# Optimization experiments

Measured on AMD Instinct MI355X. Metric: run time of the kernel, lower is better.

Reference implementation:

```python
import jax, jax.numpy as jnp
import numpy as np

N_HEAD = 9
HEAD_DIM = 64
KV_PER_HEAD = 21  # 189 // 9
ROPE_BASE = 10000.0


def _rotate_half(x):
    # matches torch: x1 = first half (floor), x2 = rest; cat(-x2, x1)
    h = x.shape[-1] // 2
    return jnp.concatenate([-x[..., h:], x[..., :h]], axis=-1)


def _rope_cos_sin(T, dtype):
    inv_freq = 1.0 / (ROPE_BASE ** (jnp.arange(0, KV_PER_HEAD, 2, dtype=jnp.float32) / KV_PER_HEAD))  # [11]
    t = jnp.arange(T, dtype=jnp.float32)
    freqs = jnp.einsum('i,j->ij', t, inv_freq)          # [T, 11]
    emb = jnp.concatenate([freqs, freqs], axis=-1)      # [T, 22]
    cos = jnp.cos(emb)[:, :KV_PER_HEAD].astype(dtype)   # [T, 21]
    sin = jnp.sin(emb)[:, :KV_PER_HEAD].astype(dtype)
    return cos, sin


def setup_inputs() -> dict:
    key = jax.random.key(0)
    ks = jax.random.split(key, 5)
    B, T, C = 4, 2048, 576
    kv_dim = 189
    s = 0.02
    return {
        'x': jax.random.normal(ks[0], (B, T, C), dtype=jnp.float32),
        'Wq': jax.random.normal(ks[1], (C, C), dtype=jnp.float32) * s,
        'Wk': jax.random.normal(ks[2], (C, kv_dim), dtype=jnp.float32) * s,
        'Wv': jax.random.normal(ks[3], (C, kv_dim), dtype=jnp.float32) * s,
        'Wo': jax.random.normal(ks[4], (C, C), dtype=jnp.float32) * s,
    }


def reference(x, Wq, Wk, Wv, Wo):
    B, T, C = x.shape
    q = (x @ Wq).reshape(B, T, N_HEAD, HEAD_DIM).transpose(0, 2, 1, 3)      # [B,H,T,64]
    k = (x @ Wk).reshape(B, T, N_HEAD, KV_PER_HEAD).transpose(0, 2, 1, 3)   # [B,H,T,21]
    v = (x @ Wv).reshape(B, T, N_HEAD, KV_PER_HEAD).transpose(0, 2, 1, 3)   # [B,H,T,21]

    cos, sin = _rope_cos_sin(T, x.dtype)  # [T,21] each, broadcasts over B,H
    k_rot = k * cos + _rotate_half(k) * sin
    q_part = q[..., :KV_PER_HEAD]
    q_rot_part = q_part * cos + _rotate_half(q_part) * sin
    # q dims >= KV_PER_HEAD never touch nonzero K, so only the first 21 dims matter
    scale = 1.0 / np.sqrt(HEAD_DIM)
    scores = jnp.einsum('bhqd,bhkd->bhqk', q_rot_part, k_rot) * scale       # [B,H,T,T]
    causal = jnp.tril(jnp.ones((T, T), dtype=bool))
    scores = jnp.where(causal, scores, -1e9)
    attn = jax.nn.softmax(scores, axis=-1)
    y_small = jnp.einsum('bhqk,bhkd->bhqd', attn, v)                        # [B,H,T,21]
    # zero-pad up to head_dim (matches k_pad/v_pad construction)
    y = jnp.pad(y_small, ((0, 0), (0, 0), (0, 0), (0, HEAD_DIM - KV_PER_HEAD)))
    y = y.transpose(0, 2, 1, 3).reshape(B, T, C)
    return y @ Wo
```

## Files before the change

kernel.cpp:

```cpp
#include <hip/hip_runtime.h>
#include <hip/hip_bf16.h>

typedef unsigned short u16;
typedef unsigned int u32;
typedef __attribute__((ext_vector_type(8))) short bf16x8;
typedef __attribute__((ext_vector_type(4))) float f32x4;
typedef __attribute__((ext_vector_type(4))) int i32x4;

#define N_HEADS 9
#define T_SEQ 2048
#define BATCH 4
#define CDIM 576
#define ROWS (BATCH * T_SEQ)
#define NBH (BATCH * N_HEADS)
#define PART_SLOT ((size_t)NBH * T_SEQ * 32)

__device__ __forceinline__ u16 f2bf(float f) {
    u32 u = __float_as_uint(f);
    u32 r = u + 0x7FFFu + ((u >> 16) & 1u);
    return (u16)(r >> 16);
}
__device__ __forceinline__ float bf2f(u16 u) { return __uint_as_float(((u32)u) << 16); }
__device__ __forceinline__ u32 cvt_pk_bf16(float lo, float hi) {
    u32 r;
    asm("v_cvt_pk_bf16_f32 %0, %1, %2" : "=v"(r) : "v"(lo), "v"(hi));
    return r;
}
__device__ __forceinline__ float exp2_raw(float x) {
    float r;
    asm("v_exp_f32 %0, %1" : "=v"(r) : "v"(x));
    return r;
}

__global__ __launch_bounds__(256) void prep_wt(const float* __restrict__ Wq, const float* __restrict__ Wk,
                                               const float* __restrict__ Wv, const float* __restrict__ Wo,
                                               u16* __restrict__ WcT, u16* __restrict__ WoSubT,
                                               float* __restrict__ cosT, float* __restrict__ sinT) {
    int idx = blockIdx.x * 256 + threadIdx.x;
    if (idx < 576 * 576) {
        int n = idx / 576, k = idx - n * 576;
        float v;
        if (n < 189)      v = Wq[(size_t)k * 576 + (n / 21) * 64 + (n % 21)];
        else if (n < 378) v = Wk[(size_t)k * 189 + (n - 189)];
        else if (n < 567) v = Wv[(size_t)k * 189 + (n - 378)];
        else              v = 0.f;
        WcT[(size_t)n * 576 + k] = f2bf(v);
    }
    if (idx < 576 * 192) {
        int n = idx / 192, k = idx - n * 192;
        float v = 0.f;
        if (k < 189) v = Wo[(size_t)((k / 21) * 64 + (k % 21)) * 576 + n];
        WoSubT[(size_t)n * 192 + k] = f2bf(v);
    }
    if (idx < T_SEQ * 21) {
        int t = idx / 21, d = idx - t * 21;
        int i = (d < 11) ? d : d - 11;
        float e = (2.0f * (float)i) / 21.0f;
        float invf = exp2f(-e * 13.287712379549449f);
        float ang = (float)t * invf;
        cosT[idx] = cosf(ang);
        sinT[idx] = sinf(ang);
    }
}


template <int AF32, int OUTF32>
__global__ __launch_bounds__(256) void gemm_mfma(const void* __restrict__ Av, const u16* __restrict__ BT,
                                                 void* __restrict__ Cout, int K, int lda, int ldbt, int ldc) {
    __shared__ u16 As[128][32];
    __shared__ u16 Bs[64][32];
    const int tid = threadIdx.x;
    const int lane = tid & 63, w = tid >> 6;
    const int m0 = (blockIdx.x & 63) * 128, n0 = (blockIdx.x >> 6) * 64;
    const int k15 = lane & 15, g = lane >> 4;

    const int arow = tid >> 1;
    const int ac0 = (tid & 1) * 2;
    const int brow = tid >> 2, bc = tid & 3;

    f32x4 zero = {0.f, 0.f, 0.f, 0.f};
    f32x4 acc[2][4];
#pragma unroll
    for (int hf = 0; hf < 2; hf++)
#pragma unroll
        for (int n = 0; n < 4; n++) acc[hf][n] = zero;

    const float* Af = (const float*)Av;
    const u16*   Ab = (const u16*)Av;

    float4 af0, af1, af2, af3;
    i32x4 av0, av1;
    if (AF32) {
        const float* ap = &Af[(size_t)(m0 + arow) * lda + ac0 * 8];
        af0 = *(const float4*)&ap[0];
        af1 = *(const float4*)&ap[4];
        af2 = *(const float4*)&ap[8];
        af3 = *(const float4*)&ap[12];
    } else {
        av0 = *(const i32x4*)&Ab[(size_t)(m0 + arow) * lda + ac0 * 8];
        av1 = *(const i32x4*)&Ab[(size_t)(m0 + arow) * lda + (ac0 + 1) * 8];
    }
    i32x4 bv = *(const i32x4*)&BT[(size_t)(n0 + brow) * ldbt + bc * 8];

    for (int k0 = 0; k0 < K; k0 += 32) {
        __syncthreads();
        if (AF32) {
            i32x4 w0, w1;
            w0[0] = (int)cvt_pk_bf16(af0.x, af0.y); w0[1] = (int)cvt_pk_bf16(af0.z, af0.w);
            w0[2] = (int)cvt_pk_bf16(af1.x, af1.y); w0[3] = (int)cvt_pk_bf16(af1.z, af1.w);
            w1[0] = (int)cvt_pk_bf16(af2.x, af2.y); w1[1] = (int)cvt_pk_bf16(af2.z, af2.w);
            w1[2] = (int)cvt_pk_bf16(af3.x, af3.y); w1[3] = (int)cvt_pk_bf16(af3.z, af3.w);
            *(i32x4*)&As[arow][(ac0 ^ (arow & 3)) * 8] = w0;
            *(i32x4*)&As[arow][((ac0 + 1) ^ (arow & 3)) * 8] = w1;
        } else {
            *(i32x4*)&As[arow][(ac0 ^ (arow & 3)) * 8] = av0;
            *(i32x4*)&As[arow][((ac0 + 1) ^ (arow & 3)) * 8] = av1;
        }
        *(i32x4*)&Bs[brow][(bc ^ (brow & 3)) * 8] = bv;
        __syncthreads();
        int k1 = k0 + 32;
        if (k1 < K) {
            if (AF32) {
                const float* ap = &Af[(size_t)(m0 + arow) * lda + k1 + ac0 * 8];
                af0 = *(const float4*)&ap[0];
                af1 = *(const float4*)&ap[4];
                af2 = *(const float4*)&ap[8];
                af3 = *(const float4*)&ap[12];
            } else {
                av0 = *(const i32x4*)&Ab[(size_t)(m0 + arow) * lda + k1 + ac0 * 8];
                av1 = *(const i32x4*)&Ab[(size_t)(m0 + arow) * lda + k1 + (ac0 + 1) * 8];
            }
            bv = *(const i32x4*)&BT[(size_t)(n0 + brow) * ldbt + k1 + bc * 8];
        }
        const int ar0 = w * 32 + k15;
        bf16x8 a0 = *(const bf16x8*)&As[ar0][(g ^ (ar0 & 3)) * 8];
        bf16x8 a1 = *(const bf16x8*)&As[ar0 + 16][(g ^ (ar0 & 3)) * 8];
#pragma unroll
        for (int n = 0; n < 4; n++) {
            int br = n * 16 + k15;
            bf16x8 b = *(const bf16x8*)&Bs[br][(g ^ (br & 3)) * 8];
            acc[0][n] = __builtin_amdgcn_mfma_f32_16x16x32_bf16(a0, b, acc[0][n], 0, 0, 0);
            acc[1][n] = __builtin_amdgcn_mfma_f32_16x16x32_bf16(a1, b, acc[1][n], 0, 0, 0);
        }
    }
#pragma unroll
    for (int hf = 0; hf < 2; hf++)
#pragma unroll
        for (int n = 0; n < 4; n++)
#pragma unroll
            for (int i = 0; i < 4; i++) {
                int row = m0 + w * 32 + hf * 16 + g * 4 + i;
                int col = n0 + n * 16 + k15;
                float v = acc[hf][n][i];
                if (OUTF32) ((float*)Cout)[(size_t)row * ldc + col] = v;
                else        ((u16*)Cout)[(size_t)row * ldc + col] = f2bf(v);
            }
}


__global__ __launch_bounds__(256) void repack_qkv(const u16* __restrict__ qkv,
                                                  const float* __restrict__ cosT,
                                                  const float* __restrict__ sinT,
                                                  u16* __restrict__ Qp, u16* __restrict__ Kp,
                                                  u16* __restrict__ Vp) {
    __shared__ u16 Vs[64][26];
    const int tid = threadIdx.x;
    const int bh = blockIdx.y;
    const int b = bh / N_HEADS, h = bh - b * N_HEADS;
    const int t0 = blockIdx.x * 64;
    const int r = tid >> 2, c = tid & 3;
    const int t = t0 + r;

    const u16* qrow = qkv + (size_t)(b * T_SEQ + t) * CDIM + h * 21;
    const u16* krow = qrow + 189;
    const u16* vrow = krow + 189;

    for (int d = c * 6; d < c * 6 + 6 && d < 21; ++d) Vs[r][d] = vrow[d];

    const float* cr = cosT + t * 21;
    const float* sr = sinT + t * 21;
    u32 wq[4] = {0, 0, 0, 0}, wk[4] = {0, 0, 0, 0};
    const float sc = 0.18033688011112042f;
#pragma unroll
    for (int j = 0; j < 8; j++) {
        int d = c * 8 + j;
        float vq = 0.f, vk = 0.f;
        if (d < 21) {
            int pd = (d < 11) ? d + 10 : d - 11;
            float cc = cr[d], ss = sr[d];
            float qv = bf2f(qrow[d]), qp = bf2f(qrow[pd]);
            float kv = bf2f(krow[d]), kp = bf2f(krow[pd]);
            float rq = (d < 11) ? -qp : qp;
            float rk = (d < 11) ? -kp : kp;
            vq = (qv * cc + rq * ss) * sc;
            vk = kv * cc + rk * ss;
        }
        wq[j >> 1] |= (u32)f2bf(vq) << ((j & 1) * 16);
        wk[j >> 1] |= (u32)f2bf(vk) << ((j & 1) * 16);
    }
    size_t obase = ((size_t)bh * T_SEQ + t) * 32 + c * 8;
    i32x4 q4; q4[0] = (int)wq[0]; q4[1] = (int)wq[1]; q4[2] = (int)wq[2]; q4[3] = (int)wq[3];
    i32x4 k4; k4[0] = (int)wk[0]; k4[1] = (int)wk[1]; k4[2] = (int)wk[2]; k4[3] = (int)wk[3];
    *(i32x4*)&Qp[obase] = q4;
    *(i32x4*)&Kp[obase] = k4;

    __syncthreads();

    const int d = tid >> 3, tc = tid & 7;
    u32 wv[4];
#pragma unroll
    for (int j = 0; j < 4; j++) {
        u16 lo, hi;
        if (d < 21)      { lo = Vs[tc * 8 + j * 2][d]; hi = Vs[tc * 8 + j * 2 + 1][d]; }
        else if (d == 31){ lo = 0x3F80; hi = 0x3F80; }
        else             { lo = 0; hi = 0; }
        wv[j] = (u32)lo | ((u32)hi << 16);
    }
    i32x4 v4; v4[0] = (int)wv[0]; v4[1] = (int)wv[1]; v4[2] = (int)wv[2]; v4[3] = (int)wv[3];
    *(i32x4*)&Vp[((size_t)bh * 32 + d) * T_SEQ + t0 + tc * 8] = v4;
}


__global__ __launch_bounds__(256) void attn_mfma(const u16* __restrict__ Qp,
                                                 const u16* __restrict__ Kp,
                                                 const u16* __restrict__ Vp,
                                                 u16* __restrict__ Ybuf,
                                                 u16* __restrict__ Part) {
    __shared__ u16 Ks[128][40];
    __shared__ u16 Vt[32][136];
    __shared__ u16 Pt[4][16][72];
    const int tid = threadIdx.x;
    const int lane = tid & 63, w = tid >> 6;
    const int bh = blockIdx.y;
    const int b = bh / N_HEADS, h = bh - b * N_HEADS;
    const int k15 = lane & 15, g = lane >> 4;

    int bx = blockIdx.x, qt, ci;
    if (bx < 32)      { qt = 31 - (bx >> 2); ci = bx & 3; }
    else if (bx < 56) { int r = bx - 32; int q3 = r / 3; qt = 23 - q3; ci = r - q3 * 3; }
    else if (bx < 72) { int r = bx - 56; qt = 15 - (r >> 1); ci = r & 1; }
    else              { qt = 79 - bx; ci = 0; }
    const int q0 = qt * 64;
    const int n128 = (qt + 2) >> 1;
    const int nc = (qt >> 3) + 1;
    const int u_begin = (ci * n128) / nc;
    const int u_end = ((ci + 1) * n128) / nc;

    const u16* Kg = Kp + (((size_t)bh << 11) * 32) + (tid >> 1) * 32 + (tid & 1) * 16;
    const u16* Vg = Vp + (size_t)bh * 32 * T_SEQ + (size_t)(tid >> 3) * T_SEQ + (tid & 7) * 16;
    const int krow = tid >> 1, kcc = (tid & 1) * 16;
    const int vrow = tid >> 3, vcc = (tid & 7) * 16;

    bf16x8 qf = *(const bf16x8*)&Qp[(((size_t)bh << 11) + q0 + w * 16 + k15) * 32 + g * 8];

    f32x4 y0 = {0.f, 0.f, 0.f, 0.f}, y1 = {0.f, 0.f, 0.f, 0.f};
    const int qloc = w * 16 + k15;

    u32 ko = (u32)u_begin * 4096u;
    u32 vo = (u32)u_begin * 128u;
    i32x4 ka0 = *(const i32x4*)&Kg[ko];
    i32x4 ka1 = *(const i32x4*)&Kg[ko + 8];
    i32x4 va0 = *(const i32x4*)&Vg[vo];
    i32x4 va1 = *(const i32x4*)&Vg[vo + 8];

    for (int u = u_begin; u < u_end; ++u) {
        __syncthreads();
        *(i32x4*)&Ks[krow][kcc] = ka0;
        *(i32x4*)&Ks[krow][kcc + 8] = ka1;
        *(i32x4*)&Vt[vrow][vcc] = va0;
        *(i32x4*)&Vt[vrow][vcc + 8] = va1;
        if (u + 1 < u_end) {
            ko += 4096u; vo += 128u;
            ka0 = *(const i32x4*)&Kg[ko];
            ka1 = *(const i32x4*)&Kg[ko + 8];
            va0 = *(const i32x4*)&Vg[vo];
            va1 = *(const i32x4*)&Vg[vo + 8];
        }
        __syncthreads();

#pragma unroll
        for (int sub = 0; sub < 2; ++sub) {
            const int kt64 = u * 2 + sub;
            if (kt64 <= qt) {
                f32x4 s[4];
#pragma unroll
                for (int f = 0; f < 4; f++) {
                    bf16x8 kf = *(const bf16x8*)&Ks[sub * 64 + f * 16 + k15][g * 8];
                    f32x4 z = {0.f, 0.f, 0.f, 0.f};
                    s[f] = __builtin_amdgcn_mfma_f32_16x16x32_bf16(kf, qf, z, 0, 0, 0);
                }
                if (kt64 == qt) {
#pragma unroll
                    for (int f = 0; f < 4; f++)
#pragma unroll
                        for (int i = 0; i < 4; i++)
                            if (f * 16 + g * 4 + i > qloc) s[f][i] = -16384.f;
                }
#pragma unroll
                for (int f = 0; f < 4; f++) {
                    u32 lo = cvt_pk_bf16(exp2_raw(s[f][0]), exp2_raw(s[f][1]));
                    u32 hi = cvt_pk_bf16(exp2_raw(s[f][2]), exp2_raw(s[f][3]));
                    uint2 pk; pk.x = lo; pk.y = hi;
                    *(uint2*)&Pt[w][k15][f * 16 + g * 4] = pk;
                }
                asm volatile("" ::: "memory");
#pragma unroll
                for (int kh = 0; kh < 2; kh++) {
                    bf16x8 pa = *(const bf16x8*)&Pt[w][k15][kh * 32 + g * 8];
                    bf16x8 v0 = *(const bf16x8*)&Vt[k15][sub * 64 + kh * 32 + g * 8];
                    bf16x8 v1 = *(const bf16x8*)&Vt[16 + k15][sub * 64 + kh * 32 + g * 8];
                    y0 = __builtin_amdgcn_mfma_f32_16x16x32_bf16(pa, v0, y0, 0, 0, 0);
                    y1 = __builtin_amdgcn_mfma_f32_16x16x32_bf16(pa, v1, y1, 0, 0, 0);
                }
                asm volatile("" ::: "memory");
            }
        }
    }

    if (nc == 1) {
#pragma unroll
        for (int i = 0; i < 4; i++) {
            float li = __shfl(y1[i], (lane & 48) + 15);
            float inv = 1.0f / li;
            int rowY = b * T_SEQ + q0 + w * 16 + g * 4 + i;
            u16* yr = &Ybuf[(size_t)rowY * 192 + h * 21];
            yr[k15] = f2bf(y0[i] * inv);
            if (k15 < 5) yr[16 + k15] = f2bf(y1[i] * inv);
        }
    } else {
#pragma unroll
        for (int i = 0; i < 4; i++) {
            size_t pb = (size_t)ci * PART_SLOT +
                        (((size_t)bh << 11) + q0 + w * 16 + g * 4 + i) * 32;
            Part[pb + k15] = f2bf(y0[i]);
            Part[pb + 16 + k15] = f2bf(y1[i]);
        }
    }
}

__global__ __launch_bounds__(256) void attn_reduce(const u16* __restrict__ Part, u16* __restrict__ Ybuf) {
    int gid = blockIdx.x * 256 + threadIdx.x;
    int d = gid & 31;
    int rest = gid >> 5;
    int t = 512 + (rest % 1536);
    int bh = rest / 1536;
    int b = bh / N_HEADS, h = bh - b * N_HEADS;
    int qt = t >> 6;
    int nc = (qt >> 3) + 1;
    size_t base = (((size_t)bh << 11) + t) * 32;
    float l = 0.f, v = 0.f;
    for (int ci = 0; ci < nc; ci++) {
        l += bf2f(Part[(size_t)ci * PART_SLOT + base + 31]);
        if (d < 21) v += bf2f(Part[(size_t)ci * PART_SLOT + base + d]);
    }
    if (d < 21) Ybuf[(size_t)(b * T_SEQ + t) * 192 + h * 21 + d] = f2bf(v / l);
}


extern "C" void kernel_launch(void* const* d_in, const int* in_sizes, int n_in,
                              void* d_out, int out_size, void* d_ws, size_t ws_size,
                              hipStream_t stream) {
    const float* x  = (const float*)d_in[0];
    const float* Wq = (const float*)d_in[1];
    const float* Wk = (const float*)d_in[2];
    const float* Wv = (const float*)d_in[3];
    const float* Wo = (const float*)d_in[4];
    float* out = (float*)d_out;

    char* p = (char*)d_ws;
    auto alloc = [&](size_t bytes) { char* r = p; p += (bytes + 255) & ~(size_t)255; return r; };
    u16*   QpKp   = (u16*)alloc((size_t)ROWS * CDIM * 2);
    u16*   qkv    = (u16*)alloc((size_t)ROWS * CDIM * 2);
    u16*   WcT    = (u16*)alloc((size_t)576 * 576 * 2);
    u16*   WoSubT = (u16*)alloc((size_t)576 * 192 * 2);
    float* cosT   = (float*)alloc((size_t)T_SEQ * 21 * 4);
    float* sinT   = (float*)alloc((size_t)T_SEQ * 21 * 4);
    u16*   Vp     = (u16*)alloc((size_t)NBH * 32 * T_SEQ * 2);
    u16*   Ybuf   = (u16*)alloc((size_t)ROWS * 192 * 2);
    u16*   Part   = (u16*)alloc((size_t)4 * PART_SLOT * 2);

    u16* Qp = QpKp;
    u16* Kp = QpKp + (size_t)NBH * T_SEQ * 32;

    prep_wt<<<dim3((576 * 576 + 255) / 256), dim3(256), 0, stream>>>(Wq, Wk, Wv, Wo, WcT, WoSubT, cosT, sinT);

    gemm_mfma<1, 0><<<dim3(64 * 9), dim3(256), 0, stream>>>((const void*)x, WcT, (void*)qkv, 576, 576, 576, 576);

    repack_qkv<<<dim3(T_SEQ / 64, NBH), dim3(256), 0, stream>>>(qkv, cosT, sinT, Qp, Kp, Vp);

    attn_mfma<<<dim3(80, NBH), dim3(256), 0, stream>>>(Qp, Kp, Vp, Ybuf, Part);
    attn_reduce<<<dim3(NBH * 1536 * 32 / 256), dim3(256), 0, stream>>>(Part, Ybuf);

    gemm_mfma<0, 1><<<dim3(64 * 9), dim3(256), 0, stream>>>((const void*)Ybuf, WoSubT, (void*)out, 192, 192, 192, 576);
}
```

Baseline: 92.40 us.

## Stage repack loads through LDS and interleave two key subtiles in attention

```diff
diff --git a/kernel.cpp b/kernel.cpp
--- a/kernel.cpp
+++ b/kernel.cpp
@@ -163,20 +163,34 @@
                                                   const float* __restrict__ sinT,
                                                   u16* __restrict__ Qp, u16* __restrict__ Kp,
                                                   u16* __restrict__ Vp) {
-    __shared__ u16 Vs[64][26];
+    __shared__ u16 Qs[64][40];
+    __shared__ u16 Ksh[64][40];
+    __shared__ u16 Vsh[64][40];
     const int tid = threadIdx.x;
     const int bh = blockIdx.y;
     const int b = bh / N_HEADS, h = bh - b * N_HEADS;
     const int t0 = blockIdx.x * 64;
+
+    const int qa = (h * 21) & ~7,        qoff = h * 21 - qa;
+    const int ka = (189 + h * 21) & ~7,  koff = 189 + h * 21 - ka;
+    const int va = (378 + h * 21) & ~7,  voff = 378 + h * 21 - va;
+
+#pragma unroll
+    for (int it = 0; it < 3; ++it) {
+        int idx = tid + it * 256;
+        int row = idx / 12;
+        int r12 = idx - row * 12;
+        int stream = r12 >> 2, chunk = r12 & 3;
+        int off = (stream == 0) ? qa : (stream == 1) ? ka : va;
+        const u16* src = qkv + (size_t)(b * T_SEQ + t0 + row) * CDIM + off + chunk * 8;
+        i32x4 v = *(const i32x4*)src;
+        u16* dst = (stream == 0) ? &Qs[row][0] : (stream == 1) ? &Ksh[row][0] : &Vsh[row][0];
+        *(i32x4*)&dst[chunk * 8] = v;
+    }
+    __syncthreads();
+
     const int r = tid >> 2, c = tid & 3;
     const int t = t0 + r;
-
-    const u16* qrow = qkv + (size_t)(b * T_SEQ + t) * CDIM + h * 21;
-    const u16* krow = qrow + 189;
-    const u16* vrow = krow + 189;
-
-    for (int d = c * 6; d < c * 6 + 6 && d < 21; ++d) Vs[r][d] = vrow[d];
-
     const float* cr = cosT + t * 21;
     const float* sr = sinT + t * 21;
     u32 wq[4] = {0, 0, 0, 0}, wk[4] = {0, 0, 0, 0};
@@ -188,8 +202,8 @@
         if (d < 21) {
             int pd = (d < 11) ? d + 10 : d - 11;
             float cc = cr[d], ss = sr[d];
-            float qv = bf2f(qrow[d]), qp = bf2f(qrow[pd]);
-            float kv = bf2f(krow[d]), kp = bf2f(krow[pd]);
+            float qv = bf2f(Qs[r][qoff + d]),  qp = bf2f(Qs[r][qoff + pd]);
+            float kv = bf2f(Ksh[r][koff + d]), kp = bf2f(Ksh[r][koff + pd]);
             float rq = (d < 11) ? -qp : qp;
             float rk = (d < 11) ? -kp : kp;
             vq = (qv * cc + rq * ss) * sc;
@@ -204,20 +218,18 @@
     *(i32x4*)&Qp[obase] = q4;
     *(i32x4*)&Kp[obase] = k4;
 
-    __syncthreads();
-
-    const int d = tid >> 3, tc = tid & 7;
+    const int dv = tid >> 3, tc = tid & 7;
     u32 wv[4];
 #pragma unroll
     for (int j = 0; j < 4; j++) {
         u16 lo, hi;
-        if (d < 21)      { lo = Vs[tc * 8 + j * 2][d]; hi = Vs[tc * 8 + j * 2 + 1][d]; }
-        else if (d == 31){ lo = 0x3F80; hi = 0x3F80; }
-        else             { lo = 0; hi = 0; }
+        if (dv < 21)      { lo = Vsh[tc * 8 + j * 2][voff + dv]; hi = Vsh[tc * 8 + j * 2 + 1][voff + dv]; }
+        else if (dv == 31){ lo = 0x3F80; hi = 0x3F80; }
+        else              { lo = 0; hi = 0; }
         wv[j] = (u32)lo | ((u32)hi << 16);
     }
     i32x4 v4; v4[0] = (int)wv[0]; v4[1] = (int)wv[1]; v4[2] = (int)wv[2]; v4[3] = (int)wv[3];
-    *(i32x4*)&Vp[((size_t)bh * 32 + d) * T_SEQ + t0 + tc * 8] = v4;
+    *(i32x4*)&Vp[((size_t)bh * 32 + dv) * T_SEQ + t0 + tc * 8] = v4;
 }
 
 
@@ -228,7 +240,7 @@
                                                  u16* __restrict__ Part) {
     __shared__ u16 Ks[128][40];
     __shared__ u16 Vt[32][136];
-    __shared__ u16 Pt[4][16][72];
+    __shared__ u16 Pt[2][4][16][72];
     const int tid = threadIdx.x;
     const int lane = tid & 63, w = tid >> 6;
     const int bh = blockIdx.y;
@@ -278,43 +290,76 @@
         }
         __syncthreads();
 
-#pragma unroll
-        for (int sub = 0; sub < 2; ++sub) {
-            const int kt64 = u * 2 + sub;
-            if (kt64 <= qt) {
-                f32x4 s[4];
-#pragma unroll
-                for (int f = 0; f < 4; f++) {
-                    bf16x8 kf = *(const bf16x8*)&Ks[sub * 64 + f * 16 + k15][g * 8];
-                    f32x4 z = {0.f, 0.f, 0.f, 0.f};
-                    s[f] = __builtin_amdgcn_mfma_f32_16x16x32_bf16(kf, qf, z, 0, 0, 0);
-                }
-                if (kt64 == qt) {
-#pragma unroll
-                    for (int f = 0; f < 4; f++)
-#pragma unroll
-                        for (int i = 0; i < 4; i++)
-                            if (f * 16 + g * 4 + i > qloc) s[f][i] = -16384.f;
-                }
-#pragma unroll
-                for (int f = 0; f < 4; f++) {
-                    u32 lo = cvt_pk_bf16(exp2_raw(s[f][0]), exp2_raw(s[f][1]));
-                    u32 hi = cvt_pk_bf16(exp2_raw(s[f][2]), exp2_raw(s[f][3]));
-                    uint2 pk; pk.x = lo; pk.y = hi;
-                    *(uint2*)&Pt[w][k15][f * 16 + g * 4] = pk;
-                }
-                asm volatile("" ::: "memory");
-#pragma unroll
-                for (int kh = 0; kh < 2; kh++) {
-                    bf16x8 pa = *(const bf16x8*)&Pt[w][k15][kh * 32 + g * 8];
-                    bf16x8 v0 = *(const bf16x8*)&Vt[k15][sub * 64 + kh * 32 + g * 8];
-                    bf16x8 v1 = *(const bf16x8*)&Vt[16 + k15][sub * 64 + kh * 32 + g * 8];
-                    y0 = __builtin_amdgcn_mfma_f32_16x16x32_bf16(pa, v0, y0, 0, 0, 0);
-                    y1 = __builtin_amdgcn_mfma_f32_16x16x32_bf16(pa, v1, y1, 0, 0, 0);
-                }
-                asm volatile("" ::: "memory");
+        const int kt0 = u * 2;
+        const bool has1 = (kt0 + 1 <= qt);
+
+        f32x4 s0[4], s1[4];
+#pragma unroll
+        for (int f = 0; f < 4; f++) {
+            bf16x8 kf = *(const bf16x8*)&Ks[f * 16 + k15][g * 8];
+            f32x4 z = {0.f, 0.f, 0.f, 0.f};
+            s0[f] = __builtin_amdgcn_mfma_f32_16x16x32_bf16(kf, qf, z, 0, 0, 0);
+        }
+        if (has1) {
+#pragma unroll
+            for (int f = 0; f < 4; f++) {
+                bf16x8 kf = *(const bf16x8*)&Ks[64 + f * 16 + k15][g * 8];
+                f32x4 z = {0.f, 0.f, 0.f, 0.f};
+                s1[f] = __builtin_amdgcn_mfma_f32_16x16x32_bf16(kf, qf, z, 0, 0, 0);
             }
         }
+        if (kt0 == qt) {
+#pragma unroll
+            for (int f = 0; f < 4; f++)
+#pragma unroll
+                for (int i = 0; i < 4; i++)
+                    if (f * 16 + g * 4 + i > qloc) s0[f][i] = -16384.f;
+        }
+        if (has1 && kt0 + 1 == qt) {
+#pragma unroll
+            for (int f = 0; f < 4; f++)
+#pragma unroll
+                for (int i = 0; i < 4; i++)
+                    if (f * 16 + g * 4 + i > qloc) s1[f][i] = -16384.f;
+        }
+
+#pragma unroll
+        for (int f = 0; f < 4; f++) {
+            u32 lo = cvt_pk_bf16(exp2_raw(s0[f][0]), exp2_raw(s0[f][1]));
+            u32 hi = cvt_pk_bf16(exp2_raw(s0[f][2]), exp2_raw(s0[f][3]));
+            uint2 pk; pk.x = lo; pk.y = hi;
+            *(uint2*)&Pt[0][w][k15][f * 16 + g * 4] = pk;
+        }
+        if (has1) {
+#pragma unroll
+            for (int f = 0; f < 4; f++) {
+                u32 lo = cvt_pk_bf16(exp2_raw(s1[f][0]), exp2_raw(s1[f][1]));
+                u32 hi = cvt_pk_bf16(exp2_raw(s1[f][2]), exp2_raw(s1[f][3]));
+                uint2 pk; pk.x = lo; pk.y = hi;
+                *(uint2*)&Pt[1][w][k15][f * 16 + g * 4] = pk;
+            }
+        }
+        asm volatile("" ::: "memory");
+
+#pragma unroll
+        for (int kh = 0; kh < 2; kh++) {
+            bf16x8 pa = *(const bf16x8*)&Pt[0][w][k15][kh * 32 + g * 8];
+            bf16x8 v0 = *(const bf16x8*)&Vt[k15][kh * 32 + g * 8];
+            bf16x8 v1 = *(const bf16x8*)&Vt[16 + k15][kh * 32 + g * 8];
+            y0 = __builtin_amdgcn_mfma_f32_16x16x32_bf16(pa, v0, y0, 0, 0, 0);
+            y1 = __builtin_amdgcn_mfma_f32_16x16x32_bf16(pa, v1, y1, 0, 0, 0);
+        }
+        if (has1) {
+#pragma unroll
+            for (int kh = 0; kh < 2; kh++) {
+                bf16x8 pa = *(const bf16x8*)&Pt[1][w][k15][kh * 32 + g * 8];
+                bf16x8 v0 = *(const bf16x8*)&Vt[k15][64 + kh * 32 + g * 8];
+                bf16x8 v1 = *(const bf16x8*)&Vt[16 + k15][64 + kh * 32 + g * 8];
+                y0 = __builtin_amdgcn_mfma_f32_16x16x32_bf16(pa, v0, y0, 0, 0, 0);
+                y1 = __builtin_amdgcn_mfma_f32_16x16x32_bf16(pa, v1, y1, 0, 0, 0);
+            }
+        }
+        asm volatile("" ::: "memory");
     }
 
     if (nc == 1) {
```

Result: faster. 79.83 us (-13.6%).
